# Performance work log

Hardware: AMD Instinct MI355X
Metric: run time of the kernel (lower is better)

## Reference

```python
import jax, jax.numpy as jnp
import numpy as np

B, S, D, H, MB = 2, 2048, 2048, 32, 16
HD = D // H          # 64
N = S // MB          # 128 mini-batches
EPS = 1e-5
BASE_LR = 1.0


def setup_inputs() -> dict:
    ks = jax.random.split(jax.random.key(0), 8)
    sc = 1.0 / np.sqrt(D)
    inv = 1.0 / (10000.0 ** (np.arange(0, HD, 2, dtype=np.float64) / HD))
    return {
        "x": jax.random.normal(ks[0], (B, S, D), jnp.float32),
        "pos_frequencies": jnp.asarray(np.outer(np.arange(S), inv), jnp.float32),  # (S, HD//2) rope angles
        "Wq": jax.random.normal(ks[1], (D, D), jnp.float32) * sc,
        "Wk": jax.random.normal(ks[2], (D, D), jnp.float32) * sc,
        "Wv": jax.random.normal(ks[3], (D, D), jnp.float32) * sc,
        "Wo": jax.random.normal(ks[4], (D, D), jnp.float32) * sc,
        "post_gamma": jnp.ones((D,), jnp.float32),
        "post_beta": jnp.zeros((D,), jnp.float32),
        "ilr_W": jax.random.normal(ks[5], (H, 1, D), jnp.float32) * 0.02,  # inner_loop_lr_W
        "ilr_b": jnp.zeros((H, 1), jnp.float32),                            # inner_loop_lr_b
        "lgs": jnp.zeros((MB,), jnp.float32),                               # learnable_gradient_scale
        "ttt_gamma": jnp.ones((H, HD), jnp.float32),                        # ttt_norm_weight
        "ttt_beta": jnp.zeros((H, HD), jnp.float32),                        # ttt_norm_bias
        "W0": jax.random.normal(ks[6], (H, HD, HD), jnp.float32) / np.sqrt(HD),
        "b0": jnp.zeros((H, 1, HD), jnp.float32),
    }


def _rope(x, freqs):
    # x: (B,H,S,HD), freqs: (S,HD//2); rotate interleaved pairs
    cos = jnp.cos(freqs)[None, None]
    sin = jnp.sin(freqs)[None, None]
    x1, x2 = x[..., 0::2], x[..., 1::2]
    return jnp.stack([x1 * cos - x2 * sin, x1 * sin + x2 * cos], -1).reshape(x.shape)


def _ln_fwd(z, g, b):
    mu = z.mean(-1, keepdims=True)
    var = z.var(-1, keepdims=True)
    return g * (z - mu) * jax.lax.rsqrt(var + EPS) + b


def _ln_l2_bwd(z, tgt, g, b):
    # grad of 0.5*||LN(z) - tgt||^2 w.r.t. z (fused LayerNorm backward)
    mu = z.mean(-1, keepdims=True)
    var = z.var(-1, keepdims=True)
    rstd = jax.lax.rsqrt(var + EPS)
    zh = (z - mu) * rstd
    dy = (g * zh + b) - tgt
    dzh = dy * g
    return (dzh - dzh.mean(-1, keepdims=True) - zh * (dzh * zh).mean(-1, keepdims=True)) * rstd


def reference(x, pos_frequencies, Wq, Wk, Wv, Wo, post_gamma, post_beta,
              ilr_W, ilr_b, lgs, ttt_gamma, ttt_beta, W0, b0):
    # projections (torch Linear: x @ W.T), shape (B,H,S,HD)
    q = (x @ Wq.T).reshape(B, S, H, HD).transpose(0, 2, 1, 3)
    k = (x @ Wk.T).reshape(B, S, H, HD).transpose(0, 2, 1, 3)
    v = (x @ Wv.T).reshape(B, S, H, HD).transpose(0, 2, 1, 3)
    q = _rope(q, pos_frequencies)
    k = _rope(k, pos_frequencies)
    v = _rope(v, pos_frequencies)  # module applies RoPE to V too

    # inner-loop learning rates: (B,H,N,1,MB), gradient_scale: (MB,1)
    xr = x.reshape(B, N, MB, D)
    lr = jnp.einsum('bnkd,hod->bhnko', xr, ilr_W) + ilr_b.reshape(1, H, 1, 1, 1)
    lr = BASE_LR * jax.nn.sigmoid(lr).transpose(0, 1, 2, 4, 3) / HD
    gs = jnp.clip(1.0 / jnp.arange(1, MB + 1, dtype=jnp.float32) + lgs, 0.0)
    eta = gs.reshape(1, 1, 1, MB, 1) * lr  # (B,H,N,MB,MB)

    to_n = lambda t: t.reshape(B, H, N, MB, -1).transpose(2, 0, 1, 3, 4)
    Qn, Kn, Vn = to_n(q), to_n(k), to_n(v)           # (N,B,H,MB,HD)
    En = eta.transpose(2, 0, 1, 3, 4)                # (N,B,H,MB,MB)

    g = ttt_gamma.reshape(1, H, 1, HD)
    be = ttt_beta.reshape(1, H, 1, HD)
    W_init = jnp.broadcast_to(W0[None], (B, H, HD, HD))
    b_init = jnp.broadcast_to(b0[None], (B, H, 1, HD))

    def step(carry, inp):
        W, bb = carry
        XQ, XK, XV, E = inp
        Z = XK @ W + bb
        grad = _ln_l2_bwd(Z, XV - XK, g, be)                 # (B,H,MB,HD)
        Attn = jnp.tril(XQ @ XK.swapaxes(-1, -2))            # causal dual form
        b_bar = bb - jnp.tril(E) @ grad
        Z_bar = XQ @ W - (E * Attn) @ grad + b_bar
        last_eta = E[..., -1, :, None]                       # (B,H,MB,1)
        W_new = W - jnp.swapaxes(last_eta * XK, -1, -2) @ grad
        b_new = bb - jnp.sum(last_eta * grad, axis=-2, keepdims=True)
        return (W_new, b_new), XQ + _ln_fwd(Z_bar, g, be)

    _, ys = jax.lax.scan(step, (W_init, b_init), (Qn, Kn, Vn, En))  # ys: (N,B,H,MB,HD)
    out = ys.transpose(1, 0, 3, 2, 4).reshape(B, S, D)

    mu = out.mean(-1, keepdims=True)
    var = out.var(-1, keepdims=True)
    out = post_gamma * (out - mu) * jax.lax.rsqrt(var + EPS) + post_beta
    return out @ Wo.T
```

## Files before the change

### kernel.cpp

```cpp
#include <hip/hip_runtime.h>
#include <hip/hip_bf16.h>
#include <math.h>

#define BB 2
#define SS 2048
#define DD 2048
#define HH 32
#define HDD 64
#define MBB 16
#define NN 128

typedef unsigned short u16;
typedef short bf16x8_t __attribute__((ext_vector_type(8)));
typedef short bf16x4_t __attribute__((ext_vector_type(4)));
typedef float f32x4_t __attribute__((ext_vector_type(4)));

__device__ __forceinline__ float b2f(u16 u) { return __uint_as_float(((unsigned)u) << 16); }
__device__ __forceinline__ u16 f2b(float f) {
    unsigned u = __float_as_uint(f);
    return (u16)((u + 0x7FFFu + ((u >> 16) & 1u)) >> 16);
}
__device__ __forceinline__ unsigned pk2(float a, float b) {
    return (unsigned)f2b(a) | ((unsigned)f2b(b) << 16);
}
__device__ __forceinline__ unsigned cvtpk(float lo, float hi) {
    unsigned r;
    asm("v_cvt_pk_bf16_f32 %0, %1, %2" : "=v"(r) : "v"(lo), "v"(hi));
    return r;
}
__device__ __forceinline__ unsigned pk2r(u16 a, u16 b) { return (unsigned)a | ((unsigned)b << 16); }
__device__ __forceinline__ bf16x4_t mk4(unsigned lo, unsigned hi) {
    union { unsigned u[2]; bf16x4_t v; } t;
    t.u[0] = lo;
    t.u[1] = hi;
    return t.v;
}
#define MFMA16(A, B, C) __builtin_amdgcn_mfma_f32_16x16x16bf16_1k((A), (B), (C), 0, 0, 0)

__device__ __forceinline__ float wsum(float x) {
    x += __shfl_xor(x, 32);
    x += __shfl_xor(x, 16);
    x += __shfl_xor(x, 8);
    x += __shfl_xor(x, 4);
    x += __shfl_xor(x, 2);
    x += __shfl_xor(x, 1);
    return x;
}

template <int CTRL>
__device__ __forceinline__ float dppadd(float x) {
    int t = __builtin_amdgcn_update_dpp(0, __float_as_int(x), CTRL, 0xF, 0xF, true);
    return x + __int_as_float(t);
}
__device__ __forceinline__ float rsum16(float x) {
    x = dppadd<0xB1>(x);
    x = dppadd<0x4E>(x);
    x = dppadd<0x141>(x);
    x = dppadd<0x140>(x);
    return x;
}

typedef __attribute__((address_space(3))) unsigned int lds_u32;
typedef __attribute__((address_space(1))) const unsigned int glb_u32;
__device__ __forceinline__ void async_copy16(const void* g, void* l) {
    __builtin_amdgcn_global_load_lds((glb_u32*)g, (lds_u32*)l, 16, 0, 0);
}


__global__ __launch_bounds__(256) void k_cvt5(const float* __restrict__ x, const float* __restrict__ wq,
                                              const float* __restrict__ wk, const float* __restrict__ wv,
                                              const float* __restrict__ wo, u16* __restrict__ xb,
                                              u16* __restrict__ wqb, u16* __restrict__ wkb,
                                              u16* __restrict__ wvb, u16* __restrict__ wob) {
    int sl = blockIdx.y;
    long e = (long)(blockIdx.x * 256 + threadIdx.x) * 4;
    if (sl == 5) {
        long n = e >> 11;
        int cin = (int)(e & 2047);
        int hd0 = (cin >> 6) * 64 + ((cin & 63) >> 2);
        const float* src = wo + n * 2048 + hd0;
        float f0 = src[0], f1 = src[16], f2 = src[32], f3 = src[48];
        uint2 o;
        o.x = pk2(f0, f1);
        o.y = pk2(f2, f3);
        *(uint2*)(wob + e) = o;
        return;
    }
    const float* s;
    u16* d;
    if (sl == 0) { s = x; d = xb; }
    else if (sl == 1) { s = x + 4194304; d = xb + 4194304; }
    else if (sl == 2) { s = wq; d = wqb; }
    else if (sl == 3) { s = wk; d = wkb; }
    else { s = wv; d = wvb; }
    float4 f = *(const float4*)(s + e);
    uint2 o;
    o.x = pk2(f.x, f.y);
    o.y = pk2(f.z, f.w);
    *(uint2*)(d + e) = o;
}

__global__ void k_trig(const float* __restrict__ pf, float* __restrict__ ct, float* __restrict__ st) {
    int i = blockIdx.x * 256 + threadIdx.x;
    float f = pf[i];
    ct[i] = cosf(f);
    st[i] = sinf(f);
}

__global__ void k_ppg(const float* __restrict__ pg, const float* __restrict__ pb,
                      float* __restrict__ pgp, float* __restrict__ pbp) {
    int i = blockIdx.x * 256 + threadIdx.x;
    int h = i >> 6, o = i & 63;
    int src = h * 64 + (o >> 2) + (o & 3) * 16;
    pgp[i] = pg[src];
    pbp[i] = pb[src];
}

template <int EPI>
__global__ __launch_bounds__(256) void k_gemm_bt(const u16* __restrict__ A, const u16* __restrict__ B0,
                                                 const u16* __restrict__ B1, const u16* __restrict__ B2,
                                                 void* __restrict__ C0, void* __restrict__ C1,
                                                 void* __restrict__ C2, int M, int Nn, int K,
                                                 const float* __restrict__ ct, const float* __restrict__ st,
                                                 u16* __restrict__ P0, u16* __restrict__ P1) {
    __shared__ u16 As[128 * 32];
    __shared__ u16 Bs[128 * 32];
    int z = blockIdx.z;
    const u16* Bm = (z == 0) ? B0 : (z == 1) ? B1 : B2;
    void* Cout = (z == 0) ? C0 : (z == 1) ? C1 : C2;
    u16* Pout = (z == 0) ? P0 : P1;
    int tid = threadIdx.x, lane = tid & 63, wv = tid >> 6;
    int m0 = blockIdx.y * 128, n0 = blockIdx.x * 128;
    int wm = wv >> 1, wn = wv & 1;

    f32x4_t acc[4][4];
    f32x4_t zero = {0.f, 0.f, 0.f, 0.f};
#pragma unroll
    for (int a = 0; a < 4; ++a)
#pragma unroll
        for (int b = 0; b < 4; ++b) acc[a][b] = zero;

    int mrow = lane & 15, qk = (lane >> 4) * 8;
    const int kTiles = K >> 5;
    for (int kt = 0; kt < kTiles; ++kt) {
        __syncthreads();
        int kb = kt << 5;
#pragma unroll
        for (int it = 0; it < 2; ++it) {
            int cb = it * 256 + wv * 64;
            int c = cb + lane;
            const u16* gpA = A + (m0 + (c >> 2)) * K + kb + ((c & 3) << 3);
            async_copy16(gpA, &As[cb << 3]);
            const u16* gpB = Bm + (n0 + (c >> 2)) * K + kb + ((c & 3) << 3);
            async_copy16(gpB, &Bs[cb << 3]);
        }
        asm volatile("s_waitcnt vmcnt(0)" ::: "memory");
        __syncthreads();

        bf16x8_t af[4], bfr[4];
#pragma unroll
        for (int mi = 0; mi < 4; ++mi)
            af[mi] = *(const bf16x8_t*)&As[(wm * 64 + mi * 16 + mrow) * 32 + qk];
#pragma unroll
        for (int ni = 0; ni < 4; ++ni)
            bfr[ni] = *(const bf16x8_t*)&Bs[(wn * 64 + ni * 16 + mrow) * 32 + qk];
#pragma unroll
        for (int mi = 0; mi < 4; ++mi)
#pragma unroll
            for (int ni = 0; ni < 4; ++ni)
                acc[mi][ni] = __builtin_amdgcn_mfma_f32_16x16x32_bf16(af[mi], bfr[ni], acc[mi][ni], 0, 0, 0);
    }

    int col16 = lane & 15, rq = (lane >> 4) * 4;
#pragma unroll
    for (int mi = 0; mi < 4; ++mi) {
#pragma unroll
        for (int ni = 0; ni < 4; ++ni) {
#pragma unroll
            for (int r = 0; r < 4; ++r) {
                int gr = m0 + wm * 64 + mi * 16 + rq + r;
                int gc = n0 + wn * 64 + ni * 16 + col16;
                float val = acc[mi][ni][r];
                if (EPI == 0) {
                    ((float*)Cout)[gr * Nn + gc] = val;
                } else {
                    int b = gr >> 11, s2 = gr & 2047, hh = gc >> 6, hd = gc & 63;
                    int fi = s2 * 32 + (hd >> 1);
                    float c = ct[fi], sn = st[fi];
                    float partner = __shfl_xor(val, 1);
                    float y = (gc & 1) ? (partner * sn + val * c) : (val * c - partner * sn);
                    u16 yb = f2b(y);
                    long rowb = (((long)(b * HH + hh) * SS) + s2) * HDD;
                    int po = (hd & 15) * 4 + (hd >> 4);
                    if (z == 2) {
                        ((u16*)Cout)[rowb + po] = yb;
                    } else {
                        ((u16*)Cout)[rowb + hd] = yb;
                        Pout[rowb + po] = yb;
                    }
                }
            }
        }
    }
}

__global__ __launch_bounds__(256) void k_lr(const u16* __restrict__ xb, const float* __restrict__ ilrW,
                                            const float* __restrict__ ilrb, float* __restrict__ lrout) {
    __shared__ u16 xr[4][2048];
    int row0 = blockIdx.x * 4;
    int tid = threadIdx.x, lane = tid & 63, wv = tid >> 6;
    const unsigned* src = (const unsigned*)(xb + row0 * 2048);
    unsigned* dst = (unsigned*)xr;
    for (int i = tid; i < 4096; i += 256) dst[i] = src[i];
    __syncthreads();
    int b = row0 >> 11, s0 = row0 & 2047;
#pragma unroll
    for (int sub = 0; sub < 8; ++sub) {
        int h = wv * 8 + sub;
        const float* wp = ilrW + h * 2048;
        float a0 = 0.f, a1 = 0.f, a2 = 0.f, a3 = 0.f;
        for (int i = 0; i < 16; ++i) {
            int idx = i * 128 + lane * 2;
            float2 w2 = *(const float2*)(wp + idx);
            unsigned p0 = *(const unsigned*)&xr[0][idx];
            unsigned p1 = *(const unsigned*)&xr[1][idx];
            unsigned p2 = *(const unsigned*)&xr[2][idx];
            unsigned p3 = *(const unsigned*)&xr[3][idx];
            a0 += b2f((u16)p0) * w2.x + b2f((u16)(p0 >> 16)) * w2.y;
            a1 += b2f((u16)p1) * w2.x + b2f((u16)(p1 >> 16)) * w2.y;
            a2 += b2f((u16)p2) * w2.x + b2f((u16)(p2 >> 16)) * w2.y;
            a3 += b2f((u16)p3) * w2.x + b2f((u16)(p3 >> 16)) * w2.y;
        }
        a0 = wsum(a0);
        a1 = wsum(a1);
        a2 = wsum(a2);
        a3 = wsum(a3);
        if (lane == 0) {
            float bv = ilrb[h];
            float* op = lrout + ((b * HH + h) * SS) + s0;
            op[0] = (1.0f / (1.0f + expf(-(a0 + bv)))) * (1.0f / 64.0f);
            op[1] = (1.0f / (1.0f + expf(-(a1 + bv)))) * (1.0f / 64.0f);
            op[2] = (1.0f / (1.0f + expf(-(a2 + bv)))) * (1.0f / 64.0f);
            op[3] = (1.0f / (1.0f + expf(-(a3 + bv)))) * (1.0f / 64.0f);
        }
    }
}

__global__ __launch_bounds__(64, 1) void k_scan(const u16* __restrict__ qb, const u16* __restrict__ kb2,
                                                const u16* __restrict__ qpc, const u16* __restrict__ kpc,
                                                const u16* __restrict__ vc, const float* __restrict__ lrbuf,
                                                const float* __restrict__ lgs, const float* __restrict__ tg,
                                                const float* __restrict__ tb, const float* __restrict__ W0,
                                                const float* __restrict__ b0, u16* __restrict__ ys) {
    __shared__ u16 WbL[64 * 72];

    const int bh = blockIdx.x, h = bh & 31, b = bh >> 5;
    const int lane = threadIdx.x & 63;
    const int quad = lane >> 4, col = lane & 15;
    const int base = bh * SS;

    float gd4[4], bd4[4], bbv[4], g2[4], gb[4];
#pragma unroll
    for (int tn = 0; tn < 4; ++tn) {
        gd4[tn] = tg[h * 64 + tn * 16 + col];
        bd4[tn] = tb[h * 64 + tn * 16 + col];
        bbv[tn] = b0[h * 64 + tn * 16 + col];
        g2[tn] = gd4[tn] * gd4[tn];
        gb[tn] = gd4[tn] * bd4[tn];
    }
    float G2m;
    {
        float s = g2[0] + g2[1] + g2[2] + g2[3];
        s = rsum16(s);
        G2m = s * (1.f / 64.f);
    }
    const float gs15 = fmaxf(1.f / 16.f + lgs[15], 0.f);
    const float inv15 = gs15 > 0.f ? 1.f / gs15 : 0.f;
    float gs4[4], ratio4[4];
#pragma unroll
    for (int r = 0; r < 4; ++r) {
        int i = quad * 4 + r;
        gs4[r] = fmaxf(1.f / (float)(i + 1) + lgs[i], 0.f);
        ratio4[r] = gs4[r] * inv15;
    }

    f32x4_t Wc[4][4];
#pragma unroll
    for (int tm = 0; tm < 4; ++tm)
#pragma unroll
        for (int tn = 0; tn < 4; ++tn)
#pragma unroll
            for (int r = 0; r < 4; ++r)
                Wc[tm][tn][r] = W0[h * 4096 + (tm * 16 + quad * 4 + r) * 64 + tn * 16 + col];

    {
        unsigned* wb32 = (unsigned*)WbL;
#pragma unroll
        for (int tn = 0; tn < 4; ++tn)
#pragma unroll
            for (int tm = 0; tm < 4; ++tm) {
                int a = (tn * 16 + col) * 36 + tm * 8 + quad * 2;
                wb32[a] = cvtpk(Wc[tm][tn][0], Wc[tm][tn][1]);
                wb32[a + 1] = cvtpk(Wc[tm][tn][2], Wc[tm][tn][3]);
            }
    }

    bf16x8_t ka[2], qa[2];
    float lr4[4];
    u16 kraw[16], vraw[16], qraw[16];
    {
        const u16* kp = kb2 + (base + col) * 64;
        const u16* qp = qb + (base + col) * 64;
#pragma unroll
        for (int kh = 0; kh < 2; ++kh) {
            ka[kh] = *(const bf16x8_t*)(kp + kh * 32 + quad * 8);
            qa[kh] = *(const bf16x8_t*)(qp + kh * 32 + quad * 8);
        }
#pragma unroll
        for (int r = 0; r < 4; ++r) lr4[r] = -gs15 * lrbuf[base + quad * 4 + r];
#pragma unroll
        for (int r = 0; r < 4; ++r) {
            long ro = (long)(base + quad * 4 + r) * 64 + col * 4;
            ushort4 tk = *(const ushort4*)(kpc + ro);
            ushort4 tv = *(const ushort4*)(vc + ro);
            ushort4 tq = *(const ushort4*)(qpc + ro);
            kraw[r] = tk.x; kraw[4 + r] = tk.y; kraw[8 + r] = tk.z; kraw[12 + r] = tk.w;
            vraw[r] = tv.x; vraw[4 + r] = tv.y; vraw[8 + r] = tv.z; vraw[12 + r] = tv.w;
            qraw[r] = tq.x; qraw[4 + r] = tq.y; qraw[8 + r] = tq.z; qraw[12 + r] = tq.w;
        }
    }

    bf16x8_t wbf[4][2];
#pragma unroll
    for (int tn = 0; tn < 4; ++tn)
#pragma unroll
        for (int kh = 0; kh < 2; ++kh)
            wbf[tn][kh] = *(const bf16x8_t*)&WbL[(tn * 16 + col) * 72 + kh * 32 + quad * 8];

    const f32x4_t zf = {0.f, 0.f, 0.f, 0.f};

    for (int n = 0; n < NN; ++n) {
        const int s0 = n * 16;

        bf16x8_t nka[2], nqa[2];
        float nlr[4];
        u16 nkraw[16], nvraw[16], nqraw[16];
        {
            const int sp = (n + 1 < NN) ? s0 + 16 : s0;
            const u16* kp = kb2 + (base + sp + col) * 64;
            const u16* qp = qb + (base + sp + col) * 64;
#pragma unroll
            for (int kh = 0; kh < 2; ++kh) {
                nka[kh] = *(const bf16x8_t*)(kp + kh * 32 + quad * 8);
                nqa[kh] = *(const bf16x8_t*)(qp + kh * 32 + quad * 8);
            }
#pragma unroll
            for (int r = 0; r < 4; ++r) nlr[r] = -gs15 * lrbuf[base + sp + quad * 4 + r];
#pragma unroll
            for (int r = 0; r < 4; ++r) {
                long ro = (long)(base + sp + quad * 4 + r) * 64 + col * 4;
                ushort4 tk = *(const ushort4*)(kpc + ro);
                ushort4 tv = *(const ushort4*)(vc + ro);
                ushort4 tq = *(const ushort4*)(qpc + ro);
                nkraw[r] = tk.x; nkraw[4 + r] = tk.y; nkraw[8 + r] = tk.z; nkraw[12 + r] = tk.w;
                nvraw[r] = tv.x; nvraw[4 + r] = tv.y; nvraw[8 + r] = tv.z; nvraw[12 + r] = tv.w;
                nqraw[r] = tq.x; nqraw[4 + r] = tq.y; nqraw[8 + r] = tq.z; nqraw[12 + r] = tq.w;
            }
        }

        f32x4_t z[4], xqw[4], attnT;
#pragma unroll
        for (int tn = 0; tn < 4; ++tn) {
            f32x4_t cb = {bbv[tn], bbv[tn], bbv[tn], bbv[tn]};
            z[tn] = __builtin_amdgcn_mfma_f32_16x16x32_bf16(ka[1], wbf[tn][1], cb, 0, 0, 0);
            z[tn] = __builtin_amdgcn_mfma_f32_16x16x32_bf16(ka[0], wbf[tn][0], z[tn], 0, 0, 0);
            xqw[tn] = __builtin_amdgcn_mfma_f32_16x16x32_bf16(qa[1], wbf[tn][1], cb, 0, 0, 0);
            xqw[tn] = __builtin_amdgcn_mfma_f32_16x16x32_bf16(qa[0], wbf[tn][0], xqw[tn], 0, 0, 0);
        }
        attnT = __builtin_amdgcn_mfma_f32_16x16x32_bf16(ka[1], qa[1], zf, 0, 0, 0);
        attnT = __builtin_amdgcn_mfma_f32_16x16x32_bf16(ka[0], qa[0], attnT, 0, 0, 0);

        float pv0 = (quad * 4 + 0 <= col) ? (1.f + attnT[0]) : 0.f;
        float pv1 = (quad * 4 + 1 <= col) ? (1.f + attnT[1]) : 0.f;
        float pv2 = (quad * 4 + 2 <= col) ? (1.f + attnT[2]) : 0.f;
        float pv3 = (quad * 4 + 3 <= col) ? (1.f + attnT[3]) : 0.f;
        bf16x4_t pa4 = mk4(cvtpk(pv0, pv1), cvtpk(pv2, pv3));

        float c1[16];
        float A1[4], A2[4], A3[4], A4[4], A5[4], A6[4];
#pragma unroll
        for (int r = 0; r < 4; ++r) { A1[r] = 0.f; A2[r] = 0.f; A3[r] = 0.f; A4[r] = 0.f; A5[r] = 0.f; A6[r] = 0.f; }
#pragma unroll
        for (int tn = 0; tn < 4; ++tn)
#pragma unroll
            for (int r = 0; r < 4; ++r) {
                float zv = z[tn][r];
                float tgt = b2f(vraw[tn * 4 + r]) - b2f(kraw[tn * 4 + r]);
                float c = gb[tn] - gd4[tn] * tgt;
                c1[tn * 4 + r] = c;
                float t = g2[tn] * zv;
                A1[r] += zv;
                A2[r] = fmaf(zv, zv, A2[r]);
                A3[r] += t;
                A4[r] = fmaf(t, zv, A4[r]);
                A5[r] = fmaf(c, zv, A5[r]);
                A6[r] += c;
            }
#pragma unroll
        for (int r = 0; r < 4; ++r) {
            A1[r] = rsum16(A1[r]);
            A2[r] = rsum16(A2[r]);
            A3[r] = rsum16(A3[r]);
            A4[r] = rsum16(A4[r]);
            A5[r] = rsum16(A5[r]);
            A6[r] = rsum16(A6[r]);
        }
        float mu4[4], rstd4[4], m1[4], m2[4], rl[4];
#pragma unroll
        for (int r = 0; r < 4; ++r) {
            float mu = A1[r] * (1.f / 64.f);
            float var = A2[r] * (1.f / 64.f) - mu * mu;
            float rstd = rsqrtf(var + 1e-5f);
            float T1m = A3[r] * (1.f / 64.f);
            float T2m = A4[r] * (1.f / 64.f);
            float T3m = A5[r] * (1.f / 64.f);
            float C1m = A6[r] * (1.f / 64.f);
            m1[r] = rstd * (T1m - mu * G2m) + C1m;
            m2[r] = rstd * rstd * (T2m - 2.f * mu * T1m + mu * mu * G2m) + rstd * (T3m - mu * C1m);
            mu4[r] = mu;
            rstd4[r] = rstd;
            rl[r] = rstd * lr4[r];
        }
        float gS[4][4];
#pragma unroll
        for (int tn = 0; tn < 4; ++tn)
#pragma unroll
            for (int r = 0; r < 4; ++r) {
                float zh = (z[tn][r] - mu4[r]) * rstd4[r];
                float dzh = fmaf(g2[tn], zh, c1[tn * 4 + r]);
                gS[tn][r] = fmaf(-m2[r], zh, dzh - m1[r]) * rl[r];
            }
        bf16x4_t gsB[4], xk4[4];
#pragma unroll
        for (int tn = 0; tn < 4; ++tn) {
            gsB[tn] = mk4(cvtpk(gS[tn][0], gS[tn][1]), cvtpk(gS[tn][2], gS[tn][3]));
            xk4[tn] = mk4(pk2r(kraw[tn * 4 + 0], kraw[tn * 4 + 1]), pk2r(kraw[tn * 4 + 2], kraw[tn * 4 + 3]));
        }

#pragma unroll
        for (int tm = 0; tm < 4; ++tm)
#pragma unroll
            for (int tn = 0; tn < 4; ++tn)
                Wc[tm][tn] = MFMA16(xk4[tm], gsB[tn], Wc[tm][tn]);
        {
            unsigned* wb32 = (unsigned*)WbL;
#pragma unroll
            for (int tn = 0; tn < 4; ++tn)
#pragma unroll
                for (int tm = 0; tm < 4; ++tm) {
                    int a = (tn * 16 + col) * 36 + tm * 8 + quad * 2;
                    wb32[a] = cvtpk(Wc[tm][tn][0], Wc[tm][tn][1]);
                    wb32[a + 1] = cvtpk(Wc[tm][tn][2], Wc[tm][tn][3]);
                }
        }

#pragma unroll
        for (int tn = 0; tn < 4; ++tn) {
            f32x4_t pg = MFMA16(pa4, gsB[tn], zf);
#pragma unroll
            for (int r = 0; r < 4; ++r) z[tn][r] = fmaf(ratio4[r], pg[r], xqw[tn][r]);
        }
#pragma unroll
        for (int r = 0; r < 4; ++r) {
            float s1 = z[0][r] + z[1][r] + z[2][r] + z[3][r];
            float s2 = z[0][r] * z[0][r] + z[1][r] * z[1][r] + z[2][r] * z[2][r] + z[3][r] * z[3][r];
            s1 = rsum16(s1);
            s2 = rsum16(s2);
            float mu = s1 * (1.f / 64.f);
            float var = s2 * (1.f / 64.f) - mu * mu;
            mu4[r] = mu;
            rstd4[r] = rsqrtf(var + 1e-5f);
        }
#pragma unroll
        for (int r = 0; r < 4; ++r) {
            float y0 = b2f(qraw[0 * 4 + r]) + gd4[0] * (z[0][r] - mu4[r]) * rstd4[r] + bd4[0];
            float y1 = b2f(qraw[1 * 4 + r]) + gd4[1] * (z[1][r] - mu4[r]) * rstd4[r] + bd4[1];
            float y2 = b2f(qraw[2 * 4 + r]) + gd4[2] * (z[2][r] - mu4[r]) * rstd4[r] + bd4[2];
            float y3 = b2f(qraw[3 * 4 + r]) + gd4[3] * (z[3][r] - mu4[r]) * rstd4[r] + bd4[3];
            uint2 po;
            po.x = cvtpk(y0, y1);
            po.y = cvtpk(y2, y3);
            *(uint2*)(ys + (long)(b * SS + s0 + quad * 4 + r) * DD + h * 64 + col * 4) = po;
        }

#pragma unroll
        for (int tn = 0; tn < 4; ++tn) {
            float c = gS[tn][0] + gS[tn][1] + gS[tn][2] + gS[tn][3];
            c += __shfl_xor(c, 16);
            c += __shfl_xor(c, 32);
            bbv[tn] += c;
        }

#pragma unroll
        for (int tn = 0; tn < 4; ++tn)
#pragma unroll
            for (int kh = 0; kh < 2; ++kh)
                wbf[tn][kh] = *(const bf16x8_t*)&WbL[(tn * 16 + col) * 72 + kh * 32 + quad * 8];

        ka[0] = nka[0]; ka[1] = nka[1];
        qa[0] = nqa[0]; qa[1] = nqa[1];
#pragma unroll
        for (int r = 0; r < 4; ++r) lr4[r] = nlr[r];
#pragma unroll
        for (int j = 0; j < 16; ++j) { kraw[j] = nkraw[j]; vraw[j] = nvraw[j]; qraw[j] = nqraw[j]; }
    }
}

__global__ __launch_bounds__(256) void k_postln(const u16* __restrict__ ys, const float* __restrict__ pg,
                                                const float* __restrict__ pb, u16* __restrict__ outb) {
    __shared__ float red[8];
    int row = blockIdx.x, tid = threadIdx.x, lane = tid & 63, wv = tid >> 6;
    const u16* rp = ys + row * 2048 + tid * 8;
    uint4 pkd = *(const uint4*)rp;
    float v[8];
    v[0] = b2f((u16)pkd.x); v[1] = b2f((u16)(pkd.x >> 16));
    v[2] = b2f((u16)pkd.y); v[3] = b2f((u16)(pkd.y >> 16));
    v[4] = b2f((u16)pkd.z); v[5] = b2f((u16)(pkd.z >> 16));
    v[6] = b2f((u16)pkd.w); v[7] = b2f((u16)(pkd.w >> 16));
    float s1 = 0.f, s2 = 0.f;
#pragma unroll
    for (int i = 0; i < 8; ++i) { s1 += v[i]; s2 += v[i] * v[i]; }
    s1 = wsum(s1);
    s2 = wsum(s2);
    if (lane == 0) {
        red[wv] = s1;
        red[wv + 4] = s2;
    }
    __syncthreads();
    float S1 = red[0] + red[1] + red[2] + red[3];
    float S2 = red[4] + red[5] + red[6] + red[7];
    float mu = S1 * (1.f / 2048), var = S2 * (1.f / 2048) - mu * mu;
    float rstd = rsqrtf(var + 1e-5f);
    const float4 g0 = *(const float4*)(pg + tid * 8);
    const float4 g1 = *(const float4*)(pg + tid * 8 + 4);
    const float4 b0v = *(const float4*)(pb + tid * 8);
    const float4 b1v = *(const float4*)(pb + tid * 8 + 4);
    float o[8];
    o[0] = g0.x * (v[0] - mu) * rstd + b0v.x;
    o[1] = g0.y * (v[1] - mu) * rstd + b0v.y;
    o[2] = g0.z * (v[2] - mu) * rstd + b0v.z;
    o[3] = g0.w * (v[3] - mu) * rstd + b0v.w;
    o[4] = g1.x * (v[4] - mu) * rstd + b1v.x;
    o[5] = g1.y * (v[5] - mu) * rstd + b1v.y;
    o[6] = g1.z * (v[6] - mu) * rstd + b1v.z;
    o[7] = g1.w * (v[7] - mu) * rstd + b1v.w;
    uint4 po;
    po.x = pk2(o[0], o[1]);
    po.y = pk2(o[2], o[3]);
    po.z = pk2(o[4], o[5]);
    po.w = pk2(o[6], o[7]);
    *(uint4*)(outb + row * 2048 + tid * 8) = po;
}

extern "C" void kernel_launch(void* const* d_in, const int* in_sizes, int n_in,
                              void* d_out, int out_size, void* d_ws, size_t ws_size,
                              hipStream_t stream) {
    const float* x = (const float*)d_in[0];
    const float* pf = (const float*)d_in[1];
    const float* Wq = (const float*)d_in[2];
    const float* Wk = (const float*)d_in[3];
    const float* Wv = (const float*)d_in[4];
    const float* Wo = (const float*)d_in[5];
    const float* pg = (const float*)d_in[6];
    const float* pb = (const float*)d_in[7];
    const float* ilrW = (const float*)d_in[8];
    const float* ilrb = (const float*)d_in[9];
    const float* lgs = (const float*)d_in[10];
    const float* tg = (const float*)d_in[11];
    const float* tb = (const float*)d_in[12];
    const float* W0 = (const float*)d_in[13];
    const float* b0 = (const float*)d_in[14];
    float* out = (float*)d_out;
    char* ws = (char*)d_ws;

    u16* xbf = (u16*)(ws + 0);
    u16* wqb = (u16*)(ws + 16777216);
    u16* wkb = (u16*)(ws + 25165824);
    u16* wvb = (u16*)(ws + 33554432);
    u16* wob = (u16*)(ws + 41943040);
    u16* qbuf = (u16*)(ws + 50331648);
    u16* kbuf = (u16*)(ws + 67108864);
    u16* vbuf = (u16*)(ws + 83886080);
    float* ct = (float*)(ws + 100663296);
    float* st = (float*)(ws + 100925440);
    float* lrb = (float*)(ws + 101187584);
    u16* ysb = (u16*)(ws + 101711872);
    float* pgp = (float*)(ws + 118489088);
    float* pbp = (float*)(ws + 118497280);
    u16* qpc = (u16*)(ws + 118505472);
    u16* kpc = (u16*)(ws + 135282688);
    u16* lnb = (u16*)(ws + 0);

    k_cvt5<<<dim3(4096, 6), 256, 0, stream>>>(x, Wq, Wk, Wv, Wo, xbf, wqb, wkb, wvb, wob);
    k_trig<<<256, 256, 0, stream>>>(pf, ct, st);
    k_ppg<<<8, 256, 0, stream>>>(pg, pb, pgp, pbp);

    k_gemm_bt<1><<<dim3(16, 32, 3), 256, 0, stream>>>(xbf, wqb, wkb, wvb, qbuf, kbuf, vbuf,
                                                      4096, 2048, 2048, ct, st, qpc, kpc);

    k_lr<<<1024, 256, 0, stream>>>(xbf, ilrW, ilrb, lrb);

    k_scan<<<64, 64, 0, stream>>>(qbuf, kbuf, qpc, kpc, vbuf, lrb, lgs, tg, tb, W0, b0, ysb);

    k_postln<<<4096, 256, 0, stream>>>(ysb, pgp, pbp, lnb);
    k_gemm_bt<0><<<dim3(16, 32, 1), 256, 0, stream>>>(lnb, wob, wob, wob, out, out, out,
                                                      4096, 2048, 2048, nullptr, nullptr, nullptr, nullptr);
}
```

Measured before the change: 706.9 us.

## Replace GEMM with 256x128 double-buffered, swizzled, interleaved-prefetch MFMA kernel

Replaces the simple 128x128 single-buffered GEMM, which waits on every K tile, with a 512-thread 256x128-tile kernel. It uses BK=64 double-buffered LDS, XOR-swizzled shared layout and async prefetch interleaved with MFMA groups under s_setprio. This targets load latency, LDS bank conflicts and low MFMA utilization in the QKV and output projections. It adds many barriers and relies on manual vmcnt accounting, which risks subtle sync bugs and pressure on registers and LDS.

```diff
diff --git a/kernel.cpp b/kernel.cpp
--- a/kernel.cpp
+++ b/kernel.cpp
@@ -36,6 +36,7 @@
     return t.v;
 }
 #define MFMA16(A, B, C) __builtin_amdgcn_mfma_f32_16x16x16bf16_1k((A), (B), (C), 0, 0, 0)
+#define MF(A, B, C) __builtin_amdgcn_mfma_f32_16x16x32_bf16((A), (B), (C), 0, 0, 0)
 
 __device__ __forceinline__ float wsum(float x) {
     x += __shfl_xor(x, 32);
@@ -116,73 +117,149 @@
     pbp[i] = pb[src];
 }
 
+#define VM2() asm volatile("s_waitcnt vmcnt(2)" ::: "memory")
+#define BARR() asm volatile("s_barrier" ::: "memory")
+#define STAGE_A(tau, hf)                                                                           \
+    {                                                                                              \
+        u16* dst = AS[(tau) & 1] + (hf) * 8192;                                                    \
+        int tc = ((tau) < kT ? (tau) : kT - 1) << 6;                                               \
+        _Pragma("unroll") for (int h2 = 0; h2 < 2; ++h2) {                                         \
+            int chb = h2 * 512 + wid * 64;                                                         \
+            int ch = chb + lane;                                                                   \
+            int r = ch >> 3, c8 = ch & 7;                                                          \
+            const u16* gp = A + (long)(m0 + (hf) * 128 + r) * K + tc + ((c8 ^ (r & 7)) << 3);      \
+            async_copy16(gp, dst + chb * 8);                                                       \
+        }                                                                                          \
+    }
+#define STAGE_B(tau, hf)                                                                           \
+    {                                                                                              \
+        u16* dst = BS[(tau) & 1] + (hf) * 4096;                                                    \
+        int tc = ((tau) < kT ? (tau) : kT - 1) << 6;                                               \
+        int chb = wid * 64;                                                                        \
+        int ch = chb + lane;                                                                       \
+        int r = ch >> 3, c8 = ch & 7;                                                              \
+        const u16* gp = Bm + (long)(n0 + (hf) * 64 + r) * K + tc + ((c8 ^ (r & 7)) << 3);          \
+        async_copy16(gp, dst + chb * 8);                                                           \
+    }
+#define LDA4(ab, miB)                                                                              \
+    _Pragma("unroll") for (int q = 0; q < 4; ++q) _Pragma("unroll") for (int ks = 0; ks < 2; ++ks) { \
+        int row = wm * 128 + ((miB) + q) * 16 + col16;                                             \
+        int off = (row * 64 + ks * 32 + quad8) ^ ((row & 7) << 3);                                 \
+        af[q][ks] = *(const bf16x8_t*)((ab) + off);                                                \
+    }
+#define LDB2(dst, bb, ni)                                                                          \
+    _Pragma("unroll") for (int ks = 0; ks < 2; ++ks) {                                             \
+        int row = wn * 32 + (ni) * 16 + col16;                                                     \
+        int off = (row * 64 + ks * 32 + quad8) ^ ((row & 7) << 3);                                 \
+        dst[ks] = *(const bf16x8_t*)((bb) + off);                                                  \
+    }
+#define MM8(mB, nI, b2)                                                                            \
+    __builtin_amdgcn_s_setprio(1);                                                                 \
+    _Pragma("unroll") for (int q = 0; q < 4; ++q) {                                                \
+        acc[(mB) + q][nI] = MF(af[q][0], b2[0], acc[(mB) + q][nI]);                                \
+        acc[(mB) + q][nI] = MF(af[q][1], b2[1], acc[(mB) + q][nI]);                                \
+    }                                                                                              \
+    __builtin_amdgcn_s_setprio(0);
+
 template <int EPI>
-__global__ __launch_bounds__(256) void k_gemm_bt(const u16* __restrict__ A, const u16* __restrict__ B0,
-                                                 const u16* __restrict__ B1, const u16* __restrict__ B2,
-                                                 void* __restrict__ C0, void* __restrict__ C1,
-                                                 void* __restrict__ C2, int M, int Nn, int K,
-                                                 const float* __restrict__ ct, const float* __restrict__ st,
-                                                 u16* __restrict__ P0, u16* __restrict__ P1) {
-    __shared__ u16 As[128 * 32];
-    __shared__ u16 Bs[128 * 32];
-    int z = blockIdx.z;
+__global__ __launch_bounds__(512, 2) void k_gemm256(const u16* __restrict__ A, const u16* __restrict__ B0,
+                                                    const u16* __restrict__ B1, const u16* __restrict__ B2,
+                                                    void* __restrict__ C0, void* __restrict__ C1,
+                                                    void* __restrict__ C2, int M, int Nn, int K,
+                                                    const float* __restrict__ ct, const float* __restrict__ st,
+                                                    u16* __restrict__ P0, u16* __restrict__ P1) {
+    __shared__ u16 AS[2][16384];
+    __shared__ u16 BS[2][8192];
+    const int z = blockIdx.z;
     const u16* Bm = (z == 0) ? B0 : (z == 1) ? B1 : B2;
     void* Cout = (z == 0) ? C0 : (z == 1) ? C1 : C2;
     u16* Pout = (z == 0) ? P0 : P1;
-    int tid = threadIdx.x, lane = tid & 63, wv = tid >> 6;
-    int m0 = blockIdx.y * 128, n0 = blockIdx.x * 128;
-    int wm = wv >> 1, wn = wv & 1;
-
-    f32x4_t acc[4][4];
+    const int tid = threadIdx.x, lane = tid & 63, wid = tid >> 6;
+    const int wm = wid >> 2, wn = wid & 3;
+    const int col16 = lane & 15, quad8 = (lane >> 4) * 8;
+    const int m0 = blockIdx.y * 256, n0 = blockIdx.x * 128;
+    const int kT = K >> 6;
+    const int ITERS = kT >> 1;
+
+    f32x4_t acc[8][2];
     f32x4_t zero = {0.f, 0.f, 0.f, 0.f};
 #pragma unroll
-    for (int a = 0; a < 4; ++a)
-#pragma unroll
-        for (int b = 0; b < 4; ++b) acc[a][b] = zero;
-
-    int mrow = lane & 15, qk = (lane >> 4) * 8;
-    const int kTiles = K >> 5;
-    for (int kt = 0; kt < kTiles; ++kt) {
-        __syncthreads();
-        int kb = kt << 5;
-#pragma unroll
-        for (int it = 0; it < 2; ++it) {
-            int cb = it * 256 + wv * 64;
-            int c = cb + lane;
-            const u16* gpA = A + (m0 + (c >> 2)) * K + kb + ((c & 3) << 3);
-            async_copy16(gpA, &As[cb << 3]);
-            const u16* gpB = Bm + (n0 + (c >> 2)) * K + kb + ((c & 3) << 3);
-            async_copy16(gpB, &Bs[cb << 3]);
-        }
-        asm volatile("s_waitcnt vmcnt(0)" ::: "memory");
-        __syncthreads();
-
-        bf16x8_t af[4], bfr[4];
-#pragma unroll
-        for (int mi = 0; mi < 4; ++mi)
-            af[mi] = *(const bf16x8_t*)&As[(wm * 64 + mi * 16 + mrow) * 32 + qk];
-#pragma unroll
-        for (int ni = 0; ni < 4; ++ni)
-            bfr[ni] = *(const bf16x8_t*)&Bs[(wn * 64 + ni * 16 + mrow) * 32 + qk];
-#pragma unroll
-        for (int mi = 0; mi < 4; ++mi)
-#pragma unroll
-            for (int ni = 0; ni < 4; ++ni)
-                acc[mi][ni] = __builtin_amdgcn_mfma_f32_16x16x32_bf16(af[mi], bfr[ni], acc[mi][ni], 0, 0, 0);
-    }
-
-    int col16 = lane & 15, rq = (lane >> 4) * 4;
-#pragma unroll
-    for (int mi = 0; mi < 4; ++mi) {
-#pragma unroll
-        for (int ni = 0; ni < 4; ++ni) {
+    for (int a = 0; a < 8; ++a) {
+        acc[a][0] = zero;
+        acc[a][1] = zero;
+    }
+    bf16x8_t af[4][2], bn0[2], bn1[2];
+
+    STAGE_A(0, 0);
+    STAGE_A(0, 1);
+    STAGE_B(0, 0);
+    STAGE_B(0, 1);
+    STAGE_A(1, 0);
+    VM2();
+    BARR();
+
+    for (int i = 0; i < ITERS; ++i) {
+        const int e = 2 * i, o = e + 1;
+        const u16* a0b = AS[0];
+        const u16* b0b = BS[0];
+        const u16* a1b = AS[1];
+        const u16* b1b = BS[1];
+        LDA4(a0b, 0);
+        LDB2(bn0, b0b, 0);
+        STAGE_A(o, 1);
+        BARR();
+        MM8(0, 0, bn0);
+        BARR();
+        LDB2(bn1, b0b, 1);
+        STAGE_B(o, 0);
+        BARR();
+        MM8(0, 1, bn1);
+        BARR();
+        LDA4(a0b, 4);
+        STAGE_B(o, 1);
+        BARR();
+        MM8(4, 1, bn1);
+        BARR();
+        STAGE_A(e + 2, 0);
+        BARR();
+        MM8(4, 0, bn0);
+        VM2();
+        BARR();
+        LDA4(a1b, 0);
+        LDB2(bn0, b1b, 0);
+        STAGE_A(e + 2, 1);
+        BARR();
+        MM8(0, 0, bn0);
+        BARR();
+        LDB2(bn1, b1b, 1);
+        STAGE_B(e + 2, 0);
+        BARR();
+        MM8(0, 1, bn1);
+        BARR();
+        LDA4(a1b, 4);
+        STAGE_B(e + 2, 1);
+        BARR();
+        MM8(4, 1, bn1);
+        BARR();
+        STAGE_A(o + 2, 0);
+        BARR();
+        MM8(4, 0, bn0);
+        VM2();
+        BARR();
+    }
+
+    int rq = (lane >> 4) * 4;
+#pragma unroll
+    for (int mi = 0; mi < 8; ++mi) {
+#pragma unroll
+        for (int ni = 0; ni < 2; ++ni) {
 #pragma unroll
             for (int r = 0; r < 4; ++r) {
-                int gr = m0 + wm * 64 + mi * 16 + rq + r;
-                int gc = n0 + wn * 64 + ni * 16 + col16;
+                int gr = m0 + wm * 128 + mi * 16 + rq + r;
+                int gc = n0 + wn * 32 + ni * 16 + col16;
                 float val = acc[mi][ni][r];
                 if (EPI == 0) {
-                    ((float*)Cout)[gr * Nn + gc] = val;
+                    ((float*)Cout)[(long)gr * Nn + gc] = val;
                 } else {
                     int b = gr >> 11, s2 = gr & 2047, hh = gc >> 6, hd = gc & 63;
                     int fi = s2 * 32 + (hd >> 1);
@@ -372,13 +449,13 @@
 #pragma unroll
         for (int tn = 0; tn < 4; ++tn) {
             f32x4_t cb = {bbv[tn], bbv[tn], bbv[tn], bbv[tn]};
-            z[tn] = __builtin_amdgcn_mfma_f32_16x16x32_bf16(ka[1], wbf[tn][1], cb, 0, 0, 0);
-            z[tn] = __builtin_amdgcn_mfma_f32_16x16x32_bf16(ka[0], wbf[tn][0], z[tn], 0, 0, 0);
-            xqw[tn] = __builtin_amdgcn_mfma_f32_16x16x32_bf16(qa[1], wbf[tn][1], cb, 0, 0, 0);
-            xqw[tn] = __builtin_amdgcn_mfma_f32_16x16x32_bf16(qa[0], wbf[tn][0], xqw[tn], 0, 0, 0);
-        }
-        attnT = __builtin_amdgcn_mfma_f32_16x16x32_bf16(ka[1], qa[1], zf, 0, 0, 0);
-        attnT = __builtin_amdgcn_mfma_f32_16x16x32_bf16(ka[0], qa[0], attnT, 0, 0, 0);
+            z[tn] = MF(ka[1], wbf[tn][1], cb);
+            z[tn] = MF(ka[0], wbf[tn][0], z[tn]);
+            xqw[tn] = MF(qa[1], wbf[tn][1], cb);
+            xqw[tn] = MF(qa[0], wbf[tn][0], xqw[tn]);
+        }
+        attnT = MF(ka[1], qa[1], zf);
+        attnT = MF(ka[0], qa[0], attnT);
 
         float pv0 = (quad * 4 + 0 <= col) ? (1.f + attnT[0]) : 0.f;
         float pv1 = (quad * 4 + 1 <= col) ? (1.f + attnT[1]) : 0.f;
@@ -605,7 +682,7 @@
     k_trig<<<256, 256, 0, stream>>>(pf, ct, st);
     k_ppg<<<8, 256, 0, stream>>>(pg, pb, pgp, pbp);
 
-    k_gemm_bt<1><<<dim3(16, 32, 3), 256, 0, stream>>>(xbf, wqb, wkb, wvb, qbuf, kbuf, vbuf,
+    k_gemm256<1><<<dim3(16, 16, 3), 512, 0, stream>>>(xbf, wqb, wkb, wvb, qbuf, kbuf, vbuf,
                                                       4096, 2048, 2048, ct, st, qpc, kpc);
 
     k_lr<<<1024, 256, 0, stream>>>(xbf, ilrW, ilrb, lrb);
@@ -613,6 +690,6 @@
     k_scan<<<64, 64, 0, stream>>>(qbuf, kbuf, qpc, kpc, vbuf, lrb, lgs, tg, tb, W0, b0, ysb);
 
     k_postln<<<4096, 256, 0, stream>>>(ysb, pgp, pbp, lnb);
-    k_gemm_bt<0><<<dim3(16, 32, 1), 256, 0, stream>>>(lnb, wob, wob, wob, out, out, out,
+    k_gemm256<0><<<dim3(16, 16, 1), 512, 0, stream>>>(lnb, wob, wob, wob, out, out, out,
                                                       4096, 2048, 2048, nullptr, nullptr, nullptr, nullptr);
 }
```

Result: no change. 702.7 us (-0.6%).
